# Kernel optimization log

Measured on AMD Instinct MI355X. Metric: run time of the kernel, lower is better.

## Reference

```python
import jax, jax.numpy as jnp
import numpy as np

N = 50000
E = 800000
IN_F, HID, OUT_F = 512, 256, 64
KEEP = 0.5  # Dropout(0.5)


def setup_inputs() -> dict:
    key = jax.random.key(0)
    ks = jax.random.split(key, 7)
    X = jax.random.normal(ks[0], (N, IN_F), dtype=jnp.float32)
    # Xavier-uniform-style init for the two layer weights
    lim1 = float(np.sqrt(6.0 / (IN_F + HID)))
    lim2 = float(np.sqrt(6.0 / (HID + OUT_F)))
    W1 = jax.random.uniform(ks[1], (IN_F, HID), jnp.float32, -lim1, lim1)
    W2 = jax.random.uniform(ks[2], (HID, OUT_F), jnp.float32, -lim2, lim2)
    a_row = jnp.sort(jax.random.randint(ks[3], (E,), 0, N)).astype(jnp.int64)
    a_col = jax.random.randint(ks[4], (E,), 0, N).astype(jnp.int64)
    a_val = jax.random.uniform(ks[5], (E,), jnp.float32)
    drop_mask = jax.random.randint(ks[6], (N, HID), 0, 2).astype(jnp.int32)
    return {"X": X, "W1": W1, "W2": W2, "a_row": a_row, "a_col": a_col,
            "a_val": a_val, "drop_mask": drop_mask}


def _spmm(a_row, a_col, a_val, dense):
    # A @ dense where A is [N, N] sparse in COO form: gather + weighted segment-sum
    msgs = a_val[:, None] * dense[a_col]          # [E, d]
    return jax.ops.segment_sum(msgs, a_row, num_segments=N)


def reference(X, W1, W2, a_row, a_col, a_val, drop_mask):
    # layer 1: feature transform + neighbor aggregation
    h = _spmm(a_row, a_col, a_val, X @ W1)        # [N, HID]
    h = jax.nn.relu(h)
    h = h * drop_mask.astype(h.dtype) * (1.0 / KEEP)  # Dropout(0.5), train mode
    # layer 2
    out = _spmm(a_row, a_col, a_val, h @ W2)      # [N, OUT_F]
    return jax.nn.log_softmax(out, axis=1)
```

## Files before the change

### kernel.cpp

```cpp
#include <hip/hip_runtime.h>
#include <hip/hip_bf16.h>
#include <math.h>

#define NN   50000
#define EE   800000
#define INF  512
#define HIDF 256
#define OUTF 64
#define MTILES (NN/16)

using short8 = __attribute__((ext_vector_type(8))) short;
using short4v = __attribute__((ext_vector_type(4))) short;
using f32x4  = __attribute__((ext_vector_type(4))) float;
using i32x4  = __attribute__((ext_vector_type(4))) int;

typedef __attribute__((address_space(1))) const void gas_void;
typedef __attribute__((address_space(3))) void las_void;

static __device__ __forceinline__ short f2bf(float f){
  unsigned u = __builtin_bit_cast(unsigned, f);
  u += 0x7fff + ((u >> 16) & 1);
  return (short)(u >> 16);
}
static __device__ __forceinline__ float bf2f(short s){
  unsigned u = ((unsigned)(unsigned short)s) << 16;
  return __builtin_bit_cast(float, u);
}

__global__ void k_prep(const int* __restrict__ a_row, int* __restrict__ row_ptr,
                       const float* __restrict__ W1, short* __restrict__ W1p,
                       const float* __restrict__ W2, short* __restrict__ W2bT,
                       const int* __restrict__ drop, unsigned short* __restrict__ dropP){
  int b = blockIdx.x, tid = threadIdx.x;
  if (b < 196){
    int i = b * 256 + tid;
    if (i > NN) return;
    int lo = 0, hi = EE;
    while (lo < hi){ int mid = (lo + hi) >> 1; if (a_row[mid] < i) lo = mid + 1; else hi = mid; }
    row_ptr[i] = lo;
  } else if (b < 708){
    int idx = (b - 196) * 256 + tid;
    int k = idx >> 8, col = idx & 255;
    int kk = k >> 5, k2 = k & 31;
    W1p[((kk << 8) + col) * 32 + k2] = f2bf(W1[idx]);
  } else if (b < 772){
    int idx = (b - 708) * 256 + tid;
    int k = idx >> 6, n = idx & 63;
    W2bT[n * HIDF + k] = f2bf(W2[idx]);
  } else {
    int w = (b - 772) * 256 + tid;
    const i32x4* dp = (const i32x4*)(drop + w * 16);
    i32x4 m0 = __builtin_nontemporal_load(dp);
    i32x4 m1 = __builtin_nontemporal_load(dp + 1);
    i32x4 m2 = __builtin_nontemporal_load(dp + 2);
    i32x4 m3 = __builtin_nontemporal_load(dp + 3);
    unsigned bits =
        (unsigned)(m0[0] & 1)        | ((unsigned)(m0[1] & 1) << 1)  |
        ((unsigned)(m0[2] & 1) << 2) | ((unsigned)(m0[3] & 1) << 3)  |
        ((unsigned)(m1[0] & 1) << 4) | ((unsigned)(m1[1] & 1) << 5)  |
        ((unsigned)(m1[2] & 1) << 6) | ((unsigned)(m1[3] & 1) << 7)  |
        ((unsigned)(m2[0] & 1) << 8) | ((unsigned)(m2[1] & 1) << 9)  |
        ((unsigned)(m2[2] & 1) << 10)| ((unsigned)(m2[3] & 1) << 11) |
        ((unsigned)(m3[0] & 1) << 12)| ((unsigned)(m3[1] & 1) << 13) |
        ((unsigned)(m3[2] & 1) << 14)| ((unsigned)(m3[3] & 1) << 15);
    dropP[w] = (unsigned short)bits;
  }
}

__global__ __launch_bounds__(256) void k_gemm1(const float* __restrict__ X,
                                               const short* __restrict__ W1p,
                                               short* __restrict__ XW1b){
  __shared__ short lds[2][256 * 32];
  int wave = threadIdx.x >> 6, lane = threadIdx.x & 63;
  int l16 = lane & 15, quad = lane >> 4;
  int m0 = blockIdx.x * 64 + wave * 16;
  int r = min(m0 + l16, NN - 1);
  const f32x4* ap = (const f32x4*)(X + (size_t)r * INF + quad * 8);

  f32x4 acc[16];
  #pragma unroll
  for (int t = 0; t < 16; t++) acc[t] = (f32x4){0.f,0.f,0.f,0.f};

  auto stage = [&](int buf, int kk){
    const char* src = (const char*)(W1p + kk * (256 * 32));
    char* dst = (char*)&lds[buf][0];
    #pragma unroll
    for (int j = 0; j < 4; j++){
      int off = wave * 4096 + j * 1024;
      __builtin_amdgcn_global_load_lds((gas_void*)(src + off + lane * 16),
                                       (las_void*)(dst + off), 16, 0, 0);
    }
  };

  stage(0, 0);
  f32x4 a0 = __builtin_nontemporal_load(ap);
  f32x4 a1 = __builtin_nontemporal_load(ap + 1);
  __syncthreads();

  for (int kk = 0; kk < 16; kk++){
    int cur = kk & 1;
    f32x4 na0, na1;
    if (kk < 15){
      stage(cur ^ 1, kk + 1);
      na0 = __builtin_nontemporal_load(ap + (kk + 1) * 8);
      na1 = __builtin_nontemporal_load(ap + (kk + 1) * 8 + 1);
    }
    short8 af;
    af[0]=f2bf(a0[0]); af[1]=f2bf(a0[1]); af[2]=f2bf(a0[2]); af[3]=f2bf(a0[3]);
    af[4]=f2bf(a1[0]); af[5]=f2bf(a1[1]); af[6]=f2bf(a1[2]); af[7]=f2bf(a1[3]);
    const short* bp = &lds[cur][0] + l16 * 32 + quad * 8;
    #pragma unroll
    for (int nt = 0; nt < 16; nt++){
      short8 bf = *(const short8*)(bp + nt * 512);
      acc[nt] = __builtin_amdgcn_mfma_f32_16x16x32_bf16(af, bf, acc[nt], 0, 0, 0);
    }
    a0 = na0; a1 = na1;
    __syncthreads();
  }

  #pragma unroll
  for (int nt = 0; nt < 16; nt++){
    int col = nt*16 + l16;
    #pragma unroll
    for (int rr = 0; rr < 4; rr++){
      int row = m0 + quad*4 + rr;
      if (row < NN) XW1b[(size_t)row * HIDF + col] = f2bf(acc[nt][rr]);
    }
  }
}

__global__ __launch_bounds__(256) void k_spmm1(const int* __restrict__ row_ptr,
                                               const int* __restrict__ a_col,
                                               const float* __restrict__ a_val,
                                               const short* __restrict__ XW1b,
                                               const unsigned short* __restrict__ dropP,
                                               short* __restrict__ hb){
  int wave = threadIdx.x >> 6, lane = threadIdx.x & 63;
  int r = blockIdx.x * 4 + wave;
  int s = row_ptr[r], e = row_ptr[r+1];
  int g = lane >> 4;
  int c16 = lane & 15;
  int d = e - s;

  int   lim = d < 64 ? d : 64;
  bool  lv  = lane < lim;
  float myv = lv ? a_val[s + lane] : 0.f;
  int   myc = lv ? a_col[s + lane] : 0;

  float acc[16];
  #pragma unroll
  for (int j = 0; j < 16; j++) acc[j] = 0.f;

  int nsteps = (lim + 3) >> 2;
  for (int t = 0; t < nsteps; t += 2){
    int e0 = 4*t + g, e1 = 4*t + 4 + g;
    float v0 = __shfl(myv, e0);  int c0 = __shfl(myc, e0);
    float v1 = __shfl(myv, e1);  int c1 = __shfl(myc, e1);
    const short* p0 = XW1b + (c0 << 8) + c16 * 16;
    const short* p1 = XW1b + (c1 << 8) + c16 * 16;
    short8 xa0 = *(const short8*)(p0), xb0 = *(const short8*)(p0 + 8);
    short8 xa1 = *(const short8*)(p1), xb1 = *(const short8*)(p1 + 8);
    #pragma unroll
    for (int j = 0; j < 8; j++){
      acc[j]   += v0 * bf2f(xa0[j]);  acc[j+8] += v0 * bf2f(xb0[j]);
      acc[j]   += v1 * bf2f(xa1[j]);  acc[j+8] += v1 * bf2f(xb1[j]);
    }
  }
  if (d > 64){
    for (int i = s + 64 + g; i < e; i += 4){
      float v = a_val[i];  int c = a_col[i];
      const short* p = XW1b + (c << 8) + c16 * 16;
      short8 xa = *(const short8*)(p), xb = *(const short8*)(p + 8);
      #pragma unroll
      for (int j = 0; j < 8; j++){
        acc[j] += v * bf2f(xa[j]);  acc[j+8] += v * bf2f(xb[j]);
      }
    }
  }

  #pragma unroll
  for (int j = 0; j < 16; j++){
    acc[j] += __shfl_xor(acc[j], 16);
    acc[j] += __shfl_xor(acc[j], 32);
  }
  if (lane < 16){
    unsigned bits = dropP[r * 16 + c16];
    short8 o0, o1;
    #pragma unroll
    for (int j = 0; j < 8; j++){
      o0[j] = f2bf(fmaxf(acc[j],   0.f) * (((bits >> j)     & 1) ? 2.0f : 0.0f));
      o1[j] = f2bf(fmaxf(acc[j+8], 0.f) * (((bits >> (j+8)) & 1) ? 2.0f : 0.0f));
    }
    short* hp = hb + (size_t)r * HIDF + c16 * 16;
    *(short8*)(hp)     = o0;
    *(short8*)(hp + 8) = o1;
  }
}

__global__ __launch_bounds__(256) void k_gemm2(const short* __restrict__ A,
                                               const short* __restrict__ BT,
                                               short* __restrict__ C){
  int wave = threadIdx.x >> 6, lane = threadIdx.x & 63;
  int tile_m = blockIdx.x * 4 + wave;
  if (tile_m >= MTILES) return;
  int m0 = tile_m * 16, l16 = lane & 15, quad = lane >> 4;

  f32x4 acc[4];
  #pragma unroll
  for (int t = 0; t < 4; t++) acc[t] = (f32x4){0.f,0.f,0.f,0.f};

  const short8* ar = (const short8*)(A + (size_t)(m0 + l16) * HIDF + quad * 8);
  for (int kk = 0; kk < HIDF/32; kk++){
    short8 af = __builtin_nontemporal_load(ar + kk * 4);
    #pragma unroll
    for (int nt = 0; nt < 4; nt++){
      short8 bf = *(const short8*)(BT + (size_t)(nt*16 + l16) * HIDF + kk*32 + quad*8);
      acc[nt] = __builtin_amdgcn_mfma_f32_16x16x32_bf16(af, bf, acc[nt], 0, 0, 0);
    }
  }
  #pragma unroll
  for (int nt = 0; nt < 4; nt++){
    int col = nt*16 + l16;
    #pragma unroll
    for (int r = 0; r < 4; r++)
      C[(size_t)(m0 + quad*4 + r) * OUTF + col] = f2bf(acc[nt][r]);
  }
}

__global__ __launch_bounds__(256) void k_spmm2_lsm(const int* __restrict__ row_ptr,
                                                   const int* __restrict__ a_col,
                                                   const float* __restrict__ a_val,
                                                   const short* __restrict__ HW2b,
                                                   float* __restrict__ out){
  int wave = threadIdx.x >> 6, lane = threadIdx.x & 63;
  int r = blockIdx.x * 4 + wave;
  int s = row_ptr[r], e = row_ptr[r+1];
  int g = lane >> 4;
  int c4 = lane & 15;
  int d = e - s;

  int   lim = d < 64 ? d : 64;
  bool  lv  = lane < lim;
  float myv = lv ? a_val[s + lane] : 0.f;
  int   myc = lv ? a_col[s + lane] : 0;

  float acc[4] = {0,0,0,0};

  int nsteps = (lim + 3) >> 2;
  for (int t = 0; t < nsteps; t += 2){
    int e0 = 4*t + g, e1 = 4*t + 4 + g;
    float v0 = __shfl(myv, e0);  int c0 = __shfl(myc, e0);
    float v1 = __shfl(myv, e1);  int c1 = __shfl(myc, e1);
    short4v x0 = *(const short4v*)(HW2b + (c0 << 6) + c4 * 4);
    short4v x1 = *(const short4v*)(HW2b + (c1 << 6) + c4 * 4);
    #pragma unroll
    for (int j = 0; j < 4; j++){
      acc[j] += v0 * bf2f(x0[j]);
      acc[j] += v1 * bf2f(x1[j]);
    }
  }
  if (d > 64){
    for (int i = s + 64 + g; i < e; i += 4){
      float v = a_val[i];  int c = a_col[i];
      short4v x = *(const short4v*)(HW2b + (c << 6) + c4 * 4);
      #pragma unroll
      for (int j = 0; j < 4; j++) acc[j] += v * bf2f(x[j]);
    }
  }

  #pragma unroll
  for (int j = 0; j < 4; j++){
    acc[j] += __shfl_xor(acc[j], 16);
    acc[j] += __shfl_xor(acc[j], 32);
  }
  float m = fmaxf(fmaxf(acc[0], acc[1]), fmaxf(acc[2], acc[3]));
  #pragma unroll
  for (int o = 1; o <= 8; o <<= 1) m = fmaxf(m, __shfl_xor(m, o));
  float ssum = expf(acc[0]-m) + expf(acc[1]-m) + expf(acc[2]-m) + expf(acc[3]-m);
  #pragma unroll
  for (int o = 1; o <= 8; o <<= 1) ssum += __shfl_xor(ssum, o);
  float ls = logf(ssum);
  if (lane < 16){
    float4 o4 = { acc[0]-m-ls, acc[1]-m-ls, acc[2]-m-ls, acc[3]-m-ls };
    *(float4*)(out + (size_t)r * OUTF + c4 * 4) = o4;
  }
}

extern "C" void kernel_launch(void* const* d_in, const int* in_sizes, int n_in,
                              void* d_out, int out_size, void* d_ws, size_t ws_size,
                              hipStream_t stream) {
  const float* X      = (const float*)d_in[0];
  const float* W1     = (const float*)d_in[1];
  const float* W2     = (const float*)d_in[2];
  const int*   a_row  = (const int*)d_in[3];
  const int*   a_col  = (const int*)d_in[4];
  const float* a_val  = (const float*)d_in[5];
  const int*   drop   = (const int*)d_in[6];
  float*       out    = (float*)d_out;

  char* ws = (char*)d_ws;
  int*            row_ptr = (int*)           (ws);
  short*          W1p     = (short*)         (ws + 200704);
  short*          W2bT    = (short*)         (ws + 462848);
  short*          XW1b    = (short*)         (ws + 495616);
  short*          hb      = (short*)         (ws + 26095616);
  short*          HW2b    = (short*)         (ws + 51695616);
  unsigned short* dropP   = (unsigned short*)(ws + 58095616);

  k_prep<<<3897, 256, 0, stream>>>(a_row, row_ptr, W1, W1p, W2, W2bT, drop, dropP);
  k_gemm1<<<(NN + 63)/64, 256, 0, stream>>>(X, W1p, XW1b);
  k_spmm1<<<NN/4, 256, 0, stream>>>(row_ptr, a_col, a_val, XW1b, dropP, hb);
  k_gemm2<<<(MTILES + 3)/4, 256, 0, stream>>>(hb, W2bT, HW2b);
  k_spmm2_lsm<<<NN/4, 256, 0, stream>>>(row_ptr, a_col, a_val, HW2b, out);
}
```

Before: 325.7 us.

## Triple-buffer gemm1 W1 staging and widen spmm2 gathers to 16-byte loads

The first GEMM kernel moves from double to triple buffering of W1 panels in LDS, prefetching two panels ahead. Each iteration now needs one explicit vmcnt wait and one barrier instead of two __syncthreads, with the loop fully unrolled. The second SpMM kernel has each lane gather 8 bf16 values (16 bytes) instead of 4, so 8 edges are processed per step and the reduction and log-softmax code is reshaped to match. The gemm2 A-operand load drops its nontemporal hint. These trade extra LDS use and a hand-tuned wait count for fewer barriers and fewer, wider gather loads.

```diff
diff --git a/kernel.cpp b/kernel.cpp
--- a/kernel.cpp
+++ b/kernel.cpp
@@ -70,7 +70,7 @@
 __global__ __launch_bounds__(256) void k_gemm1(const float* __restrict__ X,
                                                const short* __restrict__ W1p,
                                                short* __restrict__ XW1b){
-  __shared__ short lds[2][256 * 32];
+  __shared__ short lds[3][256 * 32];
   int wave = threadIdx.x >> 6, lane = threadIdx.x & 63;
   int l16 = lane & 15, quad = lane >> 4;
   int m0 = blockIdx.x * 64 + wave * 16;
@@ -81,8 +81,8 @@
   #pragma unroll
   for (int t = 0; t < 16; t++) acc[t] = (f32x4){0.f,0.f,0.f,0.f};
 
-  auto stage = [&](int buf, int kk){
-    const char* src = (const char*)(W1p + kk * (256 * 32));
+  auto stage = [&](int buf, int panel){
+    const char* src = (const char*)(W1p + panel * (256 * 32));
     char* dst = (char*)&lds[buf][0];
     #pragma unroll
     for (int j = 0; j < 4; j++){
@@ -92,30 +92,34 @@
     }
   };
 
+  f32x4 a0[2], a1[2];
   stage(0, 0);
-  f32x4 a0 = __builtin_nontemporal_load(ap);
-  f32x4 a1 = __builtin_nontemporal_load(ap + 1);
-  __syncthreads();
-
-  for (int kk = 0; kk < 16; kk++){
-    int cur = kk & 1;
-    f32x4 na0, na1;
-    if (kk < 15){
-      stage(cur ^ 1, kk + 1);
-      na0 = __builtin_nontemporal_load(ap + (kk + 1) * 8);
-      na1 = __builtin_nontemporal_load(ap + (kk + 1) * 8 + 1);
-    }
+  a0[0] = __builtin_nontemporal_load(ap + 0);
+  a1[0] = __builtin_nontemporal_load(ap + 1);
+  stage(1, 1);
+  a0[1] = __builtin_nontemporal_load(ap + 8);
+  a1[1] = __builtin_nontemporal_load(ap + 9);
+
+  #pragma unroll
+  for (int k = 0; k < 16; k++){
+    asm volatile("s_waitcnt vmcnt(6)");
+    __builtin_amdgcn_sched_barrier(0);
+    __builtin_amdgcn_s_barrier();
+    __builtin_amdgcn_sched_barrier(0);
+    f32x4 ca0 = a0[k & 1], ca1 = a1[k & 1];
     short8 af;
-    af[0]=f2bf(a0[0]); af[1]=f2bf(a0[1]); af[2]=f2bf(a0[2]); af[3]=f2bf(a0[3]);
-    af[4]=f2bf(a1[0]); af[5]=f2bf(a1[1]); af[6]=f2bf(a1[2]); af[7]=f2bf(a1[3]);
-    const short* bp = &lds[cur][0] + l16 * 32 + quad * 8;
+    af[0]=f2bf(ca0[0]); af[1]=f2bf(ca0[1]); af[2]=f2bf(ca0[2]); af[3]=f2bf(ca0[3]);
+    af[4]=f2bf(ca1[0]); af[5]=f2bf(ca1[1]); af[6]=f2bf(ca1[2]); af[7]=f2bf(ca1[3]);
+    int p = (k + 2 < 16) ? (k + 2) : 15;
+    stage((k + 2) % 3, p);
+    a0[k & 1] = __builtin_nontemporal_load(ap + p * 8);
+    a1[k & 1] = __builtin_nontemporal_load(ap + p * 8 + 1);
+    const short* bp = &lds[k % 3][0] + l16 * 32 + quad * 8;
     #pragma unroll
     for (int nt = 0; nt < 16; nt++){
       short8 bf = *(const short8*)(bp + nt * 512);
       acc[nt] = __builtin_amdgcn_mfma_f32_16x16x32_bf16(af, bf, acc[nt], 0, 0, 0);
     }
-    a0 = na0; a1 = na1;
-    __syncthreads();
   }
 
   #pragma unroll
@@ -209,9 +213,9 @@
   #pragma unroll
   for (int t = 0; t < 4; t++) acc[t] = (f32x4){0.f,0.f,0.f,0.f};
 
-  const short8* ar = (const short8*)(A + (size_t)(m0 + l16) * HIDF + quad * 8);
+  const short* ar = A + (size_t)(m0 + l16) * HIDF + quad * 8;
   for (int kk = 0; kk < HIDF/32; kk++){
-    short8 af = __builtin_nontemporal_load(ar + kk * 4);
+    short8 af = *(const short8*)(ar + kk * 32);
     #pragma unroll
     for (int nt = 0; nt < 4; nt++){
       short8 bf = *(const short8*)(BT + (size_t)(nt*16 + l16) * HIDF + kk*32 + quad*8);
@@ -235,8 +239,8 @@
   int wave = threadIdx.x >> 6, lane = threadIdx.x & 63;
   int r = blockIdx.x * 4 + wave;
   int s = row_ptr[r], e = row_ptr[r+1];
-  int g = lane >> 4;
-  int c4 = lane & 15;
+  int g8 = lane >> 3;
+  int c8 = lane & 7;
   int d = e - s;
 
   int   lim = d < 64 ? d : 64;
@@ -244,45 +248,55 @@
   float myv = lv ? a_val[s + lane] : 0.f;
   int   myc = lv ? a_col[s + lane] : 0;
 
-  float acc[4] = {0,0,0,0};
-
-  int nsteps = (lim + 3) >> 2;
+  float acc[8];
+  #pragma unroll
+  for (int j = 0; j < 8; j++) acc[j] = 0.f;
+
+  int nsteps = (lim + 7) >> 3;
   for (int t = 0; t < nsteps; t += 2){
-    int e0 = 4*t + g, e1 = 4*t + 4 + g;
+    int e0 = 8*t + g8, e1 = 8*t + 8 + g8;
     float v0 = __shfl(myv, e0);  int c0 = __shfl(myc, e0);
     float v1 = __shfl(myv, e1);  int c1 = __shfl(myc, e1);
-    short4v x0 = *(const short4v*)(HW2b + (c0 << 6) + c4 * 4);
-    short4v x1 = *(const short4v*)(HW2b + (c1 << 6) + c4 * 4);
-    #pragma unroll
-    for (int j = 0; j < 4; j++){
+    short8 x0 = *(const short8*)(HW2b + (c0 << 6) + c8 * 8);
+    short8 x1 = *(const short8*)(HW2b + (c1 << 6) + c8 * 8);
+    #pragma unroll
+    for (int j = 0; j < 8; j++){
       acc[j] += v0 * bf2f(x0[j]);
       acc[j] += v1 * bf2f(x1[j]);
     }
   }
   if (d > 64){
-    for (int i = s + 64 + g; i < e; i += 4){
+    for (int i = s + 64 + g8; i < e; i += 8){
       float v = a_val[i];  int c = a_col[i];
-      short4v x = *(const short4v*)(HW2b + (c << 6) + c4 * 4);
+      short8 x = *(const short8*)(HW2b + (c << 6) + c8 * 8);
       #pragma unroll
-      for (int j = 0; j < 4; j++) acc[j] += v * bf2f(x[j]);
-    }
-  }
-
-  #pragma unroll
-  for (int j = 0; j < 4; j++){
+      for (int j = 0; j < 8; j++) acc[j] += v * bf2f(x[j]);
+    }
+  }
+
+  #pragma unroll
+  for (int j = 0; j < 8; j++){
+    acc[j] += __shfl_xor(acc[j], 8);
     acc[j] += __shfl_xor(acc[j], 16);
     acc[j] += __shfl_xor(acc[j], 32);
   }
-  float m = fmaxf(fmaxf(acc[0], acc[1]), fmaxf(acc[2], acc[3]));
-  #pragma unroll
-  for (int o = 1; o <= 8; o <<= 1) m = fmaxf(m, __shfl_xor(m, o));
-  float ssum = expf(acc[0]-m) + expf(acc[1]-m) + expf(acc[2]-m) + expf(acc[3]-m);
-  #pragma unroll
-  for (int o = 1; o <= 8; o <<= 1) ssum += __shfl_xor(ssum, o);
+  float m = acc[0];
+  #pragma unroll
+  for (int j = 1; j < 8; j++) m = fmaxf(m, acc[j]);
+  #pragma unroll
+  for (int o = 1; o <= 4; o <<= 1) m = fmaxf(m, __shfl_xor(m, o));
+  float ssum = 0.f;
+  #pragma unroll
+  for (int j = 0; j < 8; j++) ssum += expf(acc[j] - m);
+  #pragma unroll
+  for (int o = 1; o <= 4; o <<= 1) ssum += __shfl_xor(ssum, o);
   float ls = logf(ssum);
-  if (lane < 16){
-    float4 o4 = { acc[0]-m-ls, acc[1]-m-ls, acc[2]-m-ls, acc[3]-m-ls };
-    *(float4*)(out + (size_t)r * OUTF + c4 * 4) = o4;
+  if (lane < 8){
+    f32x4 o0 = { acc[0]-m-ls, acc[1]-m-ls, acc[2]-m-ls, acc[3]-m-ls };
+    f32x4 o1 = { acc[4]-m-ls, acc[5]-m-ls, acc[6]-m-ls, acc[7]-m-ls };
+    float* op = out + (size_t)r * OUTF + c8 * 8;
+    *(f32x4*)(op)     = o0;
+    *(f32x4*)(op + 4) = o1;
   }
 }
 
```

Result: no change. 327.8 us (+0.6%).
